# Kernel optimization log

Measured on AMD Instinct MI355X. Metric: run time of the kernel, lower is better.

## Reference

```python
import math
import jax, jax.numpy as jnp
import numpy as np

B, S, HID, H, NREL = 4, 512, 1024, 16, 64
D = HID // H  # per-head size = 64, must equal relation embedding dim


def setup_inputs() -> dict:
    key = jax.random.key(0)
    ks = jax.random.split(key, 12)
    w = lambda k, shape: jax.random.normal(k, shape, jnp.float32) * 0.02
    return {
        "q_in": jax.random.normal(ks[0], (B, S, HID), jnp.float32),
        "k_in": jax.random.normal(ks[1], (B, S, HID), jnp.float32),
        "v_in": jax.random.normal(ks[2], (B, S, HID), jnp.float32),
        "mask": jax.random.randint(ks[3], (B, 1, S, S), 0, NREL),
        "Wq": w(ks[4], (HID, HID)), "bq": jnp.zeros((HID,), jnp.float32),
        "Wk": w(ks[5], (HID, HID)), "bk": jnp.zeros((HID,), jnp.float32),
        "Wv": w(ks[6], (HID, HID)), "bv": jnp.zeros((HID,), jnp.float32),
        "Wo": w(ks[7], (HID, HID)), "bo": jnp.zeros((HID,), jnp.float32),
        "rel_k_table": w(ks[8], (NREL, D)),
        "rel_v_table": w(ks[9], (NREL, D)),
    }


def reference(q_in, k_in, v_in, mask, Wq, bq, Wk, bk, Wv, bv, Wo, bo,
              rel_k_table, rel_v_table):
    def proj(x, W, b):  # [B,S,HID] -> [B,H,S,D]
        return (x @ W.T + b).reshape(B, S, H, D).transpose(0, 2, 1, 3)

    q = proj(q_in, Wq, bq)
    k = proj(k_in, Wk, bk)
    v = proj(v_in, Wv, bv)

    ids = mask[:, 0]                      # [B,S,S] relation ids
    rel_k = rel_k_table[ids]              # [B,S,S,D]
    rel_v = rel_v_table[ids]              # [B,S,S,D]

    scores = jnp.einsum('bhqd,bhkd->bhqk', q, k)
    scores = scores + jnp.einsum('bhqd,bqkd->bhqk', q, rel_k) / 4.0
    scores = scores / math.sqrt(float(D))

    bias = (1.0 - (mask > 0).astype(scores.dtype)) * -10000.0  # [B,1,S,S]
    probs = jax.nn.softmax(scores + bias, axis=-1)             # [B,H,S,S]

    out = jnp.einsum('bhqk,bhkd->bhqd', probs, v)
    out = out + 0.25 * jnp.einsum('bhqk,bqkd->bhqd', probs, rel_v)
    out = out.transpose(0, 2, 1, 3).reshape(B, S, HID)
    return out @ Wo.T + bo
```

## Files before the change

kernel.cpp:

```cpp
#include <hip/hip_runtime.h>


typedef __attribute__((ext_vector_type(8))) short bf16x8 __attribute__((may_alias));
typedef __attribute__((ext_vector_type(4))) float f32x4;

__device__ __forceinline__ short f2bf(float x) {
    unsigned u = __float_as_uint(x);
    u += 0x7fff + ((u >> 16) & 1);
    return (short)(u >> 16);
}

__device__ __forceinline__ float bf2f(short s) {
    return __uint_as_float(((unsigned)(unsigned short)s) << 16);
}

__device__ __forceinline__ void async16(void* lds, const void* g) {
    __builtin_amdgcn_global_load_lds(
        (const __attribute__((address_space(1))) void*)g,
        (__attribute__((address_space(3))) void*)lds, 16, 0, 0);
}

__global__ __launch_bounds__(256)
void cast_all(const float* __restrict__ x0, const float* __restrict__ x1, const float* __restrict__ x2,
              const float* __restrict__ w0, const float* __restrict__ w1,
              const float* __restrict__ w2, const float* __restrict__ w3,
              const float* __restrict__ rk, const float* __restrict__ rv,
              const int* __restrict__ mask,
              short* __restrict__ y0, short* __restrict__ y1, short* __restrict__ y2,
              short* __restrict__ u0, short* __restrict__ u1,
              short* __restrict__ u2, short* __restrict__ u3,
              short* __restrict__ rkb, short* __restrict__ rvT,
              unsigned char* __restrict__ mu8)
{
    size_t i = (size_t)blockIdx.x * 256 + threadIdx.x;
    if (i < 2621440u) {
        const float* src; short* dst; size_t off;
        if (i < 3u*524288u) {
            int s = (int)(i / 524288u); off = i % 524288u;
            src = s == 0 ? x0 : (s == 1 ? x1 : x2);
            dst = s == 0 ? y0 : (s == 1 ? y1 : y2);
        } else {
            size_t j = i - 3u*524288u;
            int s = (int)(j / 262144u); off = j % 262144u;
            src = s == 0 ? w0 : (s == 1 ? w1 : (s == 2 ? w2 : w3));
            dst = s == 0 ? u0 : (s == 1 ? u1 : (s == 2 ? u2 : u3));
        }
        float4 f = ((const float4*)src)[off];
        short4 o; o.x = f2bf(f.x); o.y = f2bf(f.y); o.z = f2bf(f.z); o.w = f2bf(f.w);
        ((short4*)dst)[off] = o;
    } else if (i < 2621440u + 1024u) {
        size_t off = i - 2621440u;
        float4 f = ((const float4*)rk)[off];
        short4 o; o.x = f2bf(f.x); o.y = f2bf(f.y); o.z = f2bf(f.z); o.w = f2bf(f.w);
        ((short4*)rkb)[off] = o;
    } else if (i < 2622464u + 1024u) {
        int m = (int)(i - 2622464u);
        int d = m >> 4, r0 = (m & 15) * 4;
        short4 o;
        o.x = f2bf(rv[(size_t)(r0 + 0) * 64 + d]);
        o.y = f2bf(rv[(size_t)(r0 + 1) * 64 + d]);
        o.z = f2bf(rv[(size_t)(r0 + 2) * 64 + d]);
        o.w = f2bf(rv[(size_t)(r0 + 3) * 64 + d]);
        *(short4*)&rvT[d * 64 + r0] = o;
    } else if (i < 2623488u + 262144u) {
        size_t m = i - 2623488u;
        int4 v = ((const int4*)mask)[m];
        uchar4 o;
        o.x = (unsigned char)v.x; o.y = (unsigned char)v.y;
        o.z = (unsigned char)v.z; o.w = (unsigned char)v.w;
        ((uchar4*)mu8)[m] = o;
    }
}

__global__ __launch_bounds__(256)
void gemm12864(const short* __restrict__ A0, const short* __restrict__ A1, const short* __restrict__ A2,
               const short* __restrict__ B0, const short* __restrict__ B1, const short* __restrict__ B2,
               const float* __restrict__ c0, const float* __restrict__ c1, const float* __restrict__ c2,
               void* __restrict__ O0, void* __restrict__ O1, void* __restrict__ O2,
               int mode)
{
    __shared__ short ldsw[2 * 12288];

    const int z = blockIdx.z;
    const short* A    = z == 0 ? A0 : (z == 1 ? A1 : A2);
    const short* Bm   = z == 0 ? B0 : (z == 1 ? B1 : B2);
    const float* bias = z == 0 ? c0 : (z == 1 ? c1 : c2);
    void*        O    = z == 0 ? O0 : (z == 1 ? O1 : O2);

    const int t = threadIdx.x;
    const int lane = t & 63, w = t >> 6;
    const int wr = w >> 1, wc = w & 1;
    const int quad = lane >> 4, cl = lane & 15;
    const int rowBase = blockIdx.y * 128;
    const int colBase = blockIdx.x * 64;
    const int gl = ((lane & 7) - (lane >> 3)) & 7;

    f32x4 acc[4][2];
#pragma unroll
    for (int i = 0; i < 4; ++i)
#pragma unroll
        for (int j = 0; j < 2; ++j) acc[i][j] = (f32x4){0.f, 0.f, 0.f, 0.f};

    const int rstage = w * 8 + (lane >> 3);
    const short* Ag = A  + (size_t)(rowBase + rstage) * 1024 + gl * 8;
    const short* Bg = Bm + (size_t)(colBase + rstage) * 1024 + gl * 8;

    {
        short* Als = ldsw;
        short* Bls = ldsw + 8192;
#pragma unroll
        for (int i = 0; i < 4; ++i)
            async16(&Als[(i * 32 + w * 8) * 64], Ag + (size_t)i * 32 * 1024);
#pragma unroll
        for (int i = 0; i < 2; ++i)
            async16(&Bls[(i * 32 + w * 8) * 64], Bg + (size_t)i * 32 * 1024);
    }

    for (int it = 0; it < 16; ++it) {
        const int cur = it & 1;
        __syncthreads();
        if (it < 15) {
            short* Als = ldsw + (cur ^ 1) * 12288;
            short* Bls = Als + 8192;
            const int k0 = (it + 1) * 64;
#pragma unroll
            for (int i = 0; i < 4; ++i)
                async16(&Als[(i * 32 + w * 8) * 64], Ag + (size_t)i * 32 * 1024 + k0);
#pragma unroll
            for (int i = 0; i < 2; ++i)
                async16(&Bls[(i * 32 + w * 8) * 64], Bg + (size_t)i * 32 * 1024 + k0);
        }
        const short* Als = ldsw + cur * 12288;
        const short* Bls = Als + 8192;
#pragma unroll
        for (int kk = 0; kk < 2; ++kk) {
            bf16x8 a[4], b[2];
#pragma unroll
            for (int mi = 0; mi < 4; ++mi) {
                int r = wr * 64 + mi * 16 + cl;
                int s = (kk * 4 + quad + r) & 7;
                a[mi] = *(const bf16x8*)&Als[r * 64 + s * 8];
            }
#pragma unroll
            for (int ni = 0; ni < 2; ++ni) {
                int r = wc * 32 + ni * 16 + cl;
                int s = (kk * 4 + quad + r) & 7;
                b[ni] = *(const bf16x8*)&Bls[r * 64 + s * 8];
            }
#pragma unroll
            for (int mi = 0; mi < 4; ++mi)
#pragma unroll
                for (int ni = 0; ni < 2; ++ni)
                    acc[mi][ni] = __builtin_amdgcn_mfma_f32_16x16x32_bf16(
                        a[mi], b[ni], acc[mi][ni], 0, 0, 0);
        }
    }

    if (mode == 0) {
#pragma unroll
        for (int mi = 0; mi < 4; ++mi)
#pragma unroll
            for (int ni = 0; ni < 2; ++ni) {
                int col = colBase + wc * 32 + ni * 16 + cl;
                float bv = bias[col];
#pragma unroll
                for (int reg = 0; reg < 4; ++reg) {
                    int row = rowBase + wr * 64 + mi * 16 + quad * 4 + reg;
                    ((float*)O)[(size_t)row * 1024 + col] = acc[mi][ni][reg] + bv;
                }
            }
        return;
    }

    __syncthreads();
    short* Tls = ldsw;
    if (z == 2) {
#pragma unroll
        for (int mi = 0; mi < 4; ++mi)
#pragma unroll
            for (int ni = 0; ni < 2; ++ni) {
                int d = wc * 32 + ni * 16 + cl;
                float bv = bias[colBase + d];
                short4 pk;
                pk.x = f2bf(acc[mi][ni][0] + bv);
                pk.y = f2bf(acc[mi][ni][1] + bv);
                pk.z = f2bf(acc[mi][ni][2] + bv);
                pk.w = f2bf(acc[mi][ni][3] + bv);
                int sl = wr * 64 + mi * 16 + quad * 4;
                *(short4*)&Tls[d * 136 + sl] = pk;
            }
        __syncthreads();
        int d = t >> 2, s0 = (t & 3) * 32;
        int bb = rowBase >> 9, sBase = rowBase & 511, hh = colBase >> 6;
        short* dst = (short*)O + (((size_t)(bb * 16 + hh) * 64 + d) << 9) + sBase + s0;
#pragma unroll
        for (int j = 0; j < 4; ++j)
            *(bf16x8*)(dst + j * 8) = *(const bf16x8*)&Tls[d * 136 + s0 + j * 8];
    } else {
#pragma unroll
        for (int mi = 0; mi < 4; ++mi)
#pragma unroll
            for (int ni = 0; ni < 2; ++ni) {
                int d = wc * 32 + ni * 16 + cl;
                float bv = bias[colBase + d];
#pragma unroll
                for (int reg = 0; reg < 4; ++reg) {
                    int sl = wr * 64 + mi * 16 + quad * 4 + reg;
                    Tls[sl * 72 + d] = f2bf(acc[mi][ni][reg] + bv);
                }
            }
        __syncthreads();
        int sl = t >> 1, half = t & 1;
        int bb = rowBase >> 9, sBase = rowBase & 511, hh = colBase >> 6;
        short* dst = (short*)O + (((size_t)(bb * 16 + hh) * 512 + sBase + sl) << 6) + half * 32;
#pragma unroll
        for (int j = 0; j < 4; ++j)
            *(bf16x8*)(dst + j * 8) = *(const bf16x8*)&Tls[sl * 72 + half * 32 + j * 8];
    }
}

#define AT_BINS 4352
#define AT_PST  13056
#define AT_SLICE 17664
#define AT_TOT  (4 * AT_SLICE)

__global__ __launch_bounds__(256)
void attn_kernel(const short* __restrict__ qg, const short* __restrict__ kg,
                 const short* __restrict__ vtg, const unsigned char* __restrict__ mu8,
                 const short* __restrict__ relkb, const short* __restrict__ relvT,
                 short* __restrict__ attn_b)
{
    __shared__ __align__(16) char pool[AT_TOT];
    const int t = threadIdx.x;
    const int lane = t & 63, w = t >> 6;
    const int quad = lane >> 4, cl = lane & 15;
    char* mypool = pool + w * AT_SLICE;
    float* qwr    = (float*)mypool;
    float* bins2  = (float*)(mypool + AT_BINS);
    short* Pst    = (short*)(mypool + AT_PST);
    short* binsBf = Pst;

    const int bid = blockIdx.x;
    const int bh = bid & 63, qq = bid >> 6;
    const int b = bh >> 4, h = bh & 15, q0 = qq * 64 + w * 16;

    const short* qbase = qg  + ((size_t)bh * 512 + q0) * 64;
    const short* kbase = kg  + (size_t)bh * 512 * 64;
    const short* vbase = vtg + (size_t)bh * 64 * 512;
    const unsigned char* mb = mu8 + (size_t)b * 512 * 512 + (size_t)q0 * 512;

    for (int i = lane; i < 2 * 16 * 68; i += 64) bins2[i] = 0.f;

    bf16x8 qa0 = *(const bf16x8*)(qbase + cl * 64 + quad * 8);
    bf16x8 qa1 = *(const bf16x8*)(qbase + cl * 64 + 32 + quad * 8);

#pragma unroll
    for (int rt = 0; rt < 4; ++rt) {
        const short* kp = relkb + (size_t)(rt * 16 + cl) * 64 + quad * 8;
        bf16x8 rb0 = *(const bf16x8*)kp;
        bf16x8 rb1 = *(const bf16x8*)(kp + 32);
        f32x4 qr = (f32x4){0.f, 0.f, 0.f, 0.f};
        qr = __builtin_amdgcn_mfma_f32_16x16x32_bf16(qa0, rb0, qr, 0, 0, 0);
        qr = __builtin_amdgcn_mfma_f32_16x16x32_bf16(qa1, rb1, qr, 0, 0, 0);
#pragma unroll
        for (int reg = 0; reg < 4; ++reg)
            qwr[(quad * 4 + reg) * 68 + rt * 16 + cl] = qr[reg];
    }

    f32x4 oacc[4];
#pragma unroll
    for (int dt = 0; dt < 4; ++dt) oacc[dt] = (f32x4){0.f, 0.f, 0.f, 0.f};
    float lpart[4] = {0.f, 0.f, 0.f, 0.f};

#pragma unroll 2
    for (int c = 0; c < 8; ++c) {
        const int k0 = c * 64;
        short* myPst = Pst + (c & 1) * 1152;

        const unsigned char* mrow = mb + cl * 512 + k0 + quad * 8;
        uint2 idA0 = *(const uint2*)(mrow);
        uint2 idA1 = *(const uint2*)(mrow + 32);

        int ids[4][4];
#pragma unroll
        for (int nt = 0; nt < 4; ++nt)
#pragma unroll
            for (int reg = 0; reg < 4; ++reg)
                ids[nt][reg] = mb[(size_t)(quad * 4 + reg) * 512 + k0 + nt * 16 + cl];

        bf16x8 vb[8];
#pragma unroll
        for (int dt = 0; dt < 4; ++dt) {
            const short* vp = vbase + (size_t)(dt * 16 + cl) * 512 + k0 + quad * 8;
            vb[dt * 2]     = *(const bf16x8*)vp;
            vb[dt * 2 + 1] = *(const bf16x8*)(vp + 32);
        }

#pragma unroll
        for (int nt = 0; nt < 4; ++nt) {
            const int kidx = k0 + nt * 16 + cl;
            const short* kp = kbase + (size_t)kidx * 64 + quad * 8;
            bf16x8 kb0 = *(const bf16x8*)kp;
            bf16x8 kb1 = *(const bf16x8*)(kp + 32);
            f32x4 s = (f32x4){0.f, 0.f, 0.f, 0.f};
            __builtin_amdgcn_s_setprio(1);
            s = __builtin_amdgcn_mfma_f32_16x16x32_bf16(qa0, kb0, s, 0, 0, 0);
            s = __builtin_amdgcn_mfma_f32_16x16x32_bf16(qa1, kb1, s, 0, 0, 0);
            __builtin_amdgcn_s_setprio(0);
#pragma unroll
            for (int reg = 0; reg < 4; ++reg) {
                int q = quad * 4 + reg;
                int id = ids[nt][reg];
                float sc = (s[reg] + 0.25f * qwr[q * 68 + id]) * 0.125f;
                float p = (id == 0) ? 0.f : __expf(sc);
                lpart[reg] += p;
                myPst[q * 72 + nt * 16 + cl] = f2bf(p);
            }
        }
        bf16x8 pa0 = *(const bf16x8*)&myPst[cl * 72 + quad * 8];
        bf16x8 pa1 = *(const bf16x8*)&myPst[cl * 72 + 32 + quad * 8];
        __builtin_amdgcn_s_setprio(1);
#pragma unroll
        for (int dt = 0; dt < 4; ++dt) {
            const short* vp0 = (const short*)&vb[dt * 2];
            oacc[dt] = __builtin_amdgcn_mfma_f32_16x16x32_bf16(pa0, vb[dt * 2],     oacc[dt], 0, 0, 0);
            oacc[dt] = __builtin_amdgcn_mfma_f32_16x16x32_bf16(pa1, vb[dt * 2 + 1], oacc[dt], 0, 0, 0);
        }
        __builtin_amdgcn_s_setprio(0);

        float* myrep = bins2 + (quad >> 1) * 1088 + cl * 68;
#pragma unroll
        for (int j = 0; j < 4; ++j) {
            atomicAdd(&myrep[(idA0.x >> (8 * j)) & 255], bf2f(pa0[j]));
            atomicAdd(&myrep[(idA0.y >> (8 * j)) & 255], bf2f(pa0[j + 4]));
            atomicAdd(&myrep[(idA1.x >> (8 * j)) & 255], bf2f(pa1[j]));
            atomicAdd(&myrep[(idA1.y >> (8 * j)) & 255], bf2f(pa1[j + 4]));
        }
    }

    float invq[4];
#pragma unroll
    for (int reg = 0; reg < 4; ++reg) {
        float l = lpart[reg];
#pragma unroll
        for (int m = 8; m >= 1; m >>= 1) l += __shfl_xor(l, m);
        invq[reg] = 1.0f / l;
    }

    {
        int q = lane >> 2, r0 = (lane & 3) * 16;
#pragma unroll
        for (int j = 0; j < 4; ++j) {
            float4 fa = *(const float4*)&bins2[q * 68 + r0 + j * 4];
            float4 fb = *(const float4*)&bins2[1088 + q * 68 + r0 + j * 4];
            short4 o;
            o.x = f2bf(fa.x + fb.x); o.y = f2bf(fa.y + fb.y);
            o.z = f2bf(fa.z + fb.z); o.w = f2bf(fa.w + fb.w);
            *(short4*)&binsBf[q * 72 + r0 + j * 4] = o;
        }
    }

    bf16x8 ba0 = *(const bf16x8*)&binsBf[cl * 72 + quad * 8];
    bf16x8 ba1 = *(const bf16x8*)&binsBf[cl * 72 + 32 + quad * 8];
#pragma unroll
    for (int dt = 0; dt < 4; ++dt) {
        const short* rp = relvT + (size_t)(dt * 16 + cl) * 64 + quad * 8;
        bf16x8 rv0 = *(const bf16x8*)rp;
        bf16x8 rv1 = *(const bf16x8*)(rp + 32);
        f32x4 racc = (f32x4){0.f, 0.f, 0.f, 0.f};
        racc = __builtin_amdgcn_mfma_f32_16x16x32_bf16(ba0, rv0, racc, 0, 0, 0);
        racc = __builtin_amdgcn_mfma_f32_16x16x32_bf16(ba1, rv1, racc, 0, 0, 0);
#pragma unroll
        for (int reg = 0; reg < 4; ++reg) {
            int q = quad * 4 + reg;
            float val = (oacc[dt][reg] + 0.25f * racc[reg]) * invq[reg];
            attn_b[(size_t)(b * 512 + q0 + q) * 1024 + h * 64 + dt * 16 + cl] = f2bf(val);
        }
    }
}

extern "C" void kernel_launch(void* const* d_in, const int* in_sizes, int n_in,
                              void* d_out, int out_size, void* d_ws, size_t ws_size,
                              hipStream_t stream)
{
    const float* q_in = (const float*)d_in[0];
    const float* k_in = (const float*)d_in[1];
    const float* v_in = (const float*)d_in[2];
    const int*   mask = (const int*)d_in[3];
    const float* Wq   = (const float*)d_in[4];
    const float* bq   = (const float*)d_in[5];
    const float* Wk   = (const float*)d_in[6];
    const float* bk   = (const float*)d_in[7];
    const float* Wv   = (const float*)d_in[8];
    const float* bv   = (const float*)d_in[9];
    const float* Wo   = (const float*)d_in[10];
    const float* bo   = (const float*)d_in[11];
    const float* relk = (const float*)d_in[12];
    const float* relv = (const float*)d_in[13];

    char* ws = (char*)d_ws;
    short* qb     = (short*)(ws);
    short* kb     = (short*)(ws + (4u  << 20));
    short* vt     = (short*)(ws + (8u  << 20));
    short* attn_b = (short*)(ws + (12u << 20));
    short* Xq     = (short*)(ws + (16u << 20));
    short* Xk     = (short*)(ws + (20u << 20));
    short* Xv     = (short*)(ws + (24u << 20));
    short* Wqb    = (short*)(ws + (28u << 20));
    short* Wkb    = (short*)(ws + (30u << 20));
    short* Wvb    = (short*)(ws + (32u << 20));
    short* Wob    = (short*)(ws + (34u << 20));
    short* relkb  = (short*)(ws + (36u << 20));
    short* relvT  = (short*)(ws + (36u << 20) + 8192);
    unsigned char* masku8 = (unsigned char*)(ws + (36u << 20) + 16384);

    cast_all<<<11272, 256, 0, stream>>>(q_in, k_in, v_in, Wq, Wk, Wv, Wo, relk, relv, mask,
                                        Xq, Xk, Xv, Wqb, Wkb, Wvb, Wob, relkb, relvT, masku8);

    gemm12864<<<dim3(16, 16, 3), 256, 0, stream>>>(
        Xq, Xk, Xv, Wqb, Wkb, Wvb, bq, bk, bv, qb, kb, vt, 1);

    attn_kernel<<<dim3(512), 256, 0, stream>>>(qb, kb, vt, masku8, relkb, relvT, attn_b);

    gemm12864<<<dim3(16, 16, 1), 256, 0, stream>>>(
        attn_b, attn_b, attn_b, Wob, Wob, Wob, bo, bo, bo,
        (void*)d_out, (void*)d_out, (void*)d_out, 0);
}
```

Baseline: 243.3 us.

## Software-pipeline K and mask-id loads across attention chunks with register double-buffering

Restructures the attention key loop so that the K tiles and relation-id mask bytes for the next 64-key chunk are loaded into a second register buffer while the current chunk is being computed. The qwr gathers for a chunk are also hoisted ahead of the score MFMAs. The launch bound now requests two blocks per multiprocessor. The aim is to hide global load latency behind MFMA and exp work, at the cost of extra register pressure from holding two K and id buffers, which may cause spills under the tighter launch bound.

```diff
diff --git a/kernel.cpp b/kernel.cpp
--- a/kernel.cpp
+++ b/kernel.cpp
@@ -224,7 +224,86 @@
 #define AT_SLICE 17664
 #define AT_TOT  (4 * AT_SLICE)
 
-__global__ __launch_bounds__(256)
+#define LOADK(DST, KOFF)                                                              \
+    {                                                                                 \
+        _Pragma("unroll")                                                             \
+        for (int nt = 0; nt < 4; ++nt) {                                              \
+            const short* kp_ = kbase + (size_t)((KOFF) + nt * 16 + cl) * 64 + quad * 8; \
+            DST[nt * 2]     = *(const bf16x8*)kp_;                                    \
+            DST[nt * 2 + 1] = *(const bf16x8*)(kp_ + 32);                             \
+        }                                                                             \
+    }
+
+#define LOADIDS(DC, DA0, DA1, KOFF)                                                  \
+    {                                                                                 \
+        _Pragma("unroll")                                                             \
+        for (int nt = 0; nt < 4; ++nt) {                                              \
+            _Pragma("unroll")                                                         \
+            for (int reg = 0; reg < 4; ++reg)                                         \
+                DC[nt * 4 + reg] =                                                    \
+                    mb[(size_t)(quad * 4 + reg) * 512 + (KOFF) + nt * 16 + cl];       \
+        }                                                                             \
+        const unsigned char* mrow_ = mb + cl * 512 + (KOFF) + quad * 8;               \
+        DA0 = *(const uint2*)(mrow_);                                                 \
+        DA1 = *(const uint2*)(mrow_ + 32);                                            \
+    }
+
+#define CHUNK(K0, KC, IC, IA0, IA1, KN, IN, IA0N, IA1N, PREF)                         \
+    {                                                                                 \
+        const int k0_ = (K0);                                                         \
+        short* myPst = Pst + ((k0_ >> 6) & 1) * 1152;                                 \
+        bf16x8 vbl[8];                                                                \
+        _Pragma("unroll")                                                             \
+        for (int dt = 0; dt < 4; ++dt) {                                              \
+            const short* vp_ = vbase + (size_t)(dt * 16 + cl) * 512 + k0_ + quad * 8; \
+            vbl[dt * 2]     = *(const bf16x8*)vp_;                                    \
+            vbl[dt * 2 + 1] = *(const bf16x8*)(vp_ + 32);                             \
+        }                                                                             \
+        if (PREF) {                                                                   \
+            LOADK(KN, k0_ + 64);                                                      \
+            LOADIDS(IN, IA0N, IA1N, k0_ + 64);                                        \
+        }                                                                             \
+        float qv[16];                                                                 \
+        _Pragma("unroll")                                                             \
+        for (int e = 0; e < 16; ++e)                                                  \
+            qv[e] = qwr[(quad * 4 + (e & 3)) * 68 + IC[e]];                           \
+        _Pragma("unroll")                                                             \
+        for (int nt = 0; nt < 4; ++nt) {                                              \
+            f32x4 s = (f32x4){0.f, 0.f, 0.f, 0.f};                                    \
+            __builtin_amdgcn_s_setprio(1);                                            \
+            s = __builtin_amdgcn_mfma_f32_16x16x32_bf16(qa0, KC[nt * 2],     s, 0, 0, 0); \
+            s = __builtin_amdgcn_mfma_f32_16x16x32_bf16(qa1, KC[nt * 2 + 1], s, 0, 0, 0); \
+            __builtin_amdgcn_s_setprio(0);                                            \
+            _Pragma("unroll")                                                         \
+            for (int reg = 0; reg < 4; ++reg) {                                       \
+                int q_ = quad * 4 + reg;                                              \
+                int id_ = IC[nt * 4 + reg];                                           \
+                float sc_ = (s[reg] + 0.25f * qv[nt * 4 + reg]) * 0.125f;             \
+                float p_ = (id_ == 0) ? 0.f : __expf(sc_);                            \
+                lpart[reg] += p_;                                                     \
+                myPst[q_ * 72 + nt * 16 + cl] = f2bf(p_);                             \
+            }                                                                         \
+        }                                                                             \
+        bf16x8 pa0 = *(const bf16x8*)&myPst[cl * 72 + quad * 8];                      \
+        bf16x8 pa1 = *(const bf16x8*)&myPst[cl * 72 + 32 + quad * 8];                 \
+        __builtin_amdgcn_s_setprio(1);                                                \
+        _Pragma("unroll")                                                             \
+        for (int dt = 0; dt < 4; ++dt) {                                              \
+            oacc[dt] = __builtin_amdgcn_mfma_f32_16x16x32_bf16(pa0, vbl[dt * 2],     oacc[dt], 0, 0, 0); \
+            oacc[dt] = __builtin_amdgcn_mfma_f32_16x16x32_bf16(pa1, vbl[dt * 2 + 1], oacc[dt], 0, 0, 0); \
+        }                                                                             \
+        __builtin_amdgcn_s_setprio(0);                                                \
+        float* myrep = bins2 + (quad >> 1) * 1088 + cl * 68;                          \
+        _Pragma("unroll")                                                             \
+        for (int j = 0; j < 4; ++j) {                                                 \
+            atomicAdd(&myrep[(IA0.x >> (8 * j)) & 255], bf2f(pa0[j]));                \
+            atomicAdd(&myrep[(IA0.y >> (8 * j)) & 255], bf2f(pa0[j + 4]));            \
+            atomicAdd(&myrep[(IA1.x >> (8 * j)) & 255], bf2f(pa1[j]));                \
+            atomicAdd(&myrep[(IA1.y >> (8 * j)) & 255], bf2f(pa1[j + 4]));            \
+        }                                                                             \
+    }
+
+__global__ __launch_bounds__(256, 2)
 void attn_kernel(const short* __restrict__ qg, const short* __restrict__ kg,
                  const short* __restrict__ vtg, const unsigned char* __restrict__ mu8,
                  const short* __restrict__ relkb, const short* __restrict__ relvT,
@@ -254,6 +333,13 @@
     bf16x8 qa0 = *(const bf16x8*)(qbase + cl * 64 + quad * 8);
     bf16x8 qa1 = *(const bf16x8*)(qbase + cl * 64 + 32 + quad * 8);
 
+    bf16x8 Ka[8], Kb[8];
+    int    Ia[16], Ib[16];
+    uint2  IaA0, IaA1, IbA0, IbA1;
+
+    LOADK(Ka, 0);
+    LOADIDS(Ia, IaA0, IaA1, 0);
+
 #pragma unroll
     for (int rt = 0; rt < 4; ++rt) {
         const short* kp = relkb + (size_t)(rt * 16 + cl) * 64 + quad * 8;
@@ -272,70 +358,10 @@
     for (int dt = 0; dt < 4; ++dt) oacc[dt] = (f32x4){0.f, 0.f, 0.f, 0.f};
     float lpart[4] = {0.f, 0.f, 0.f, 0.f};
 
-#pragma unroll 2
-    for (int c = 0; c < 8; ++c) {
-        const int k0 = c * 64;
-        short* myPst = Pst + (c & 1) * 1152;
-
-        const unsigned char* mrow = mb + cl * 512 + k0 + quad * 8;
-        uint2 idA0 = *(const uint2*)(mrow);
-        uint2 idA1 = *(const uint2*)(mrow + 32);
-
-        int ids[4][4];
-#pragma unroll
-        for (int nt = 0; nt < 4; ++nt)
-#pragma unroll
-            for (int reg = 0; reg < 4; ++reg)
-                ids[nt][reg] = mb[(size_t)(quad * 4 + reg) * 512 + k0 + nt * 16 + cl];
-
-        bf16x8 vb[8];
-#pragma unroll
-        for (int dt = 0; dt < 4; ++dt) {
-            const short* vp = vbase + (size_t)(dt * 16 + cl) * 512 + k0 + quad * 8;
-            vb[dt * 2]     = *(const bf16x8*)vp;
-            vb[dt * 2 + 1] = *(const bf16x8*)(vp + 32);
-        }
-
-#pragma unroll
-        for (int nt = 0; nt < 4; ++nt) {
-            const int kidx = k0 + nt * 16 + cl;
-            const short* kp = kbase + (size_t)kidx * 64 + quad * 8;
-            bf16x8 kb0 = *(const bf16x8*)kp;
-            bf16x8 kb1 = *(const bf16x8*)(kp + 32);
-            f32x4 s = (f32x4){0.f, 0.f, 0.f, 0.f};
-            __builtin_amdgcn_s_setprio(1);
-            s = __builtin_amdgcn_mfma_f32_16x16x32_bf16(qa0, kb0, s, 0, 0, 0);
-            s = __builtin_amdgcn_mfma_f32_16x16x32_bf16(qa1, kb1, s, 0, 0, 0);
-            __builtin_amdgcn_s_setprio(0);
-#pragma unroll
-            for (int reg = 0; reg < 4; ++reg) {
-                int q = quad * 4 + reg;
-                int id = ids[nt][reg];
-                float sc = (s[reg] + 0.25f * qwr[q * 68 + id]) * 0.125f;
-                float p = (id == 0) ? 0.f : __expf(sc);
-                lpart[reg] += p;
-                myPst[q * 72 + nt * 16 + cl] = f2bf(p);
-            }
-        }
-        bf16x8 pa0 = *(const bf16x8*)&myPst[cl * 72 + quad * 8];
-        bf16x8 pa1 = *(const bf16x8*)&myPst[cl * 72 + 32 + quad * 8];
-        __builtin_amdgcn_s_setprio(1);
-#pragma unroll
-        for (int dt = 0; dt < 4; ++dt) {
-            const short* vp0 = (const short*)&vb[dt * 2];
-            oacc[dt] = __builtin_amdgcn_mfma_f32_16x16x32_bf16(pa0, vb[dt * 2],     oacc[dt], 0, 0, 0);
-            oacc[dt] = __builtin_amdgcn_mfma_f32_16x16x32_bf16(pa1, vb[dt * 2 + 1], oacc[dt], 0, 0, 0);
-        }
-        __builtin_amdgcn_s_setprio(0);
-
-        float* myrep = bins2 + (quad >> 1) * 1088 + cl * 68;
-#pragma unroll
-        for (int j = 0; j < 4; ++j) {
-            atomicAdd(&myrep[(idA0.x >> (8 * j)) & 255], bf2f(pa0[j]));
-            atomicAdd(&myrep[(idA0.y >> (8 * j)) & 255], bf2f(pa0[j + 4]));
-            atomicAdd(&myrep[(idA1.x >> (8 * j)) & 255], bf2f(pa1[j]));
-            atomicAdd(&myrep[(idA1.y >> (8 * j)) & 255], bf2f(pa1[j + 4]));
-        }
+    for (int cc = 0; cc < 4; ++cc) {
+        const int base = cc * 128;
+        CHUNK(base,      Ka, Ia, IaA0, IaA1, Kb, Ib, IbA0, IbA1, 1);
+        CHUNK(base + 64, Kb, Ib, IbA0, IbA1, Ka, Ia, IaA0, IaA1, cc < 3);
     }
 
     float invq[4];
```

New measurement: 238.6 us. -2.0%, faster.
